# Performance work log

Measured on AMD Instinct MI355X. Metric: run time of the kernel, lower is better.

The kernel has to match this reference:

```python
import jax, jax.numpy as jnp
import numpy as np

B, D, N = 128, 2, 8192
C_CENT, K, R = 32, 32, 0.25
BOTTLE = 8
BN_EPS = 1e-5


def setup_inputs() -> dict:
    key = jax.random.key(0)
    ks = jax.random.split(key, 12)
    w = lambda k, s: jax.random.normal(k, s, dtype=jnp.float32) * 0.05
    z = lambda s: jnp.zeros(s, jnp.float32)
    o = lambda s: jnp.ones(s, jnp.float32)
    return {
        "x": jax.random.normal(ks[0], (B, D, N), dtype=jnp.float32),
        "eps": jax.random.normal(ks[1], (B, BOTTLE), dtype=jnp.float32),
        "sa_c1_w": w(ks[2], (64, D)), "sa_c1_b": z((64,)),
        "sa_bn1_g": o((64,)), "sa_bn1_b": z((64,)),
        "sa_c2_w": w(ks[3], (128, 64)), "sa_c2_b": z((128,)),
        "sa_bn2_g": o((128,)), "sa_bn2_b": z((128,)),
        "sa_c3_w": w(ks[4], (256, 128)), "sa_c3_b": z((256,)),
        "sa_bn3_g": o((256,)), "sa_bn3_b": z((256,)),
        "sa_fc1_w": w(ks[5], (1024, 256 * C_CENT)), "sa_fc1_b": z((1024,)),
        "sa_bn4_g": o((1024,)), "sa_bn4_b": z((1024,)),
        "sa_fc2_w": w(ks[6], (256, 1024)), "sa_fc2_b": z((256,)),
        "sa_bn5_g": o((256,)), "sa_bn5_b": z((256,)),
        "sa_fc3_w": w(ks[7], (BOTTLE, 256)), "sa_fc3_b": z((BOTTLE,)),
        "fce1_w": w(ks[8], (BOTTLE, BOTTLE)), "fce1_b": z((BOTTLE,)),
        "fce2_w": w(ks[9], (BOTTLE, BOTTLE)), "fce2_b": z((BOTTLE,)),
        "dfc1_w": w(ks[10], (32, BOTTLE)), "dfc1_b": z((32,)),
        "dfc2_w": w(ks[11], (128, 32)), "dfc2_b": z((128,)),
        "dfc3_w": w(jax.random.fold_in(key, 99), (512, 128)), "dfc3_b": z((512,)),
    }


def _bn2d(x, g, b):
    m = jnp.mean(x, axis=(0, 2, 3), keepdims=True)
    v = jnp.var(x, axis=(0, 2, 3), keepdims=True)
    return (x - m) * jax.lax.rsqrt(v + BN_EPS) * g[None, :, None, None] + b[None, :, None, None]


def _bn1d(x, g, b):
    m = jnp.mean(x, axis=0, keepdims=True)
    v = jnp.var(x, axis=0, keepdims=True)
    return (x - m) * jax.lax.rsqrt(v + BN_EPS) * g[None, :] + b[None, :]


def _fps(points, n_centroids):
    # points: [B, D, N]; deterministic start at index 0 (torch uses randint)
    c0 = points[:, :, 0]                                   # [B, D]
    dist0 = jnp.sum((c0[:, :, None] - points) ** 2, axis=1)  # [B, N]

    def step(dist, _):
        ind = jnp.argmax(dist, axis=1)                      # [B]
        c = jnp.take_along_axis(points, ind[:, None, None], axis=2)[:, :, 0]  # [B, D]
        dist = jnp.minimum(dist, jnp.sum((c[:, :, None] - points) ** 2, axis=1))
        return dist, c

    _, cs = jax.lax.scan(step, dist0, None, length=n_centroids - 1)  # [C-1, B, D]
    cents = jnp.concatenate([c0[None], cs], axis=0)          # [C, B, D]
    return jnp.transpose(cents, (1, 2, 0))                   # [B, D, C]


def _group_points(points):
    b, _, n = points.shape
    cents = _fps(points, C_CENT)                             # [B, D, C]
    # squared pairwise distances centroid->point: [B, C, N]
    sq = (-2.0 * jnp.einsum('bdc,bdn->bcn', cents, points)
          + jnp.sum(cents ** 2, axis=1)[:, :, None]
          + jnp.sum(points ** 2, axis=1)[:, None, :])
    idx = jnp.broadcast_to(jnp.arange(n, dtype=jnp.int32), (b, C_CENT, n))
    idx = jnp.where(sq > R * R, jnp.int32(n), idx)
    idx = jnp.sort(idx, axis=-1)[:, :, :K]                   # [B, C, K]
    first = idx[:, :, :1]
    idx = jnp.where(idx == n, first, idx)
    bidx = jnp.arange(b)[:, None, None]
    grouped = points[bidx, :, idx]                            # [B, C, K, D]
    return jnp.transpose(grouped, (0, 3, 1, 2))               # [B, D, C, K]


def reference(x, eps, sa_c1_w, sa_c1_b, sa_bn1_g, sa_bn1_b, sa_c2_w, sa_c2_b,
              sa_bn2_g, sa_bn2_b, sa_c3_w, sa_c3_b, sa_bn3_g, sa_bn3_b,
              sa_fc1_w, sa_fc1_b, sa_bn4_g, sa_bn4_b, sa_fc2_w, sa_fc2_b,
              sa_bn5_g, sa_bn5_b, sa_fc3_w, sa_fc3_b, fce1_w, fce1_b,
              fce2_w, fce2_b, dfc1_w, dfc1_b, dfc2_w, dfc2_b, dfc3_w, dfc3_b):
    b = x.shape[0]
    g = _group_points(x)                                     # [B, D, C, K]
    h = jax.nn.relu(_bn2d(jnp.einsum('bdck,od->bock', g, sa_c1_w) + sa_c1_b[None, :, None, None], sa_bn1_g, sa_bn1_b))
    h = jax.nn.relu(_bn2d(jnp.einsum('bdck,od->bock', h, sa_c2_w) + sa_c2_b[None, :, None, None], sa_bn2_g, sa_bn2_b))
    h = jax.nn.relu(_bn2d(jnp.einsum('bdck,od->bock', h, sa_c3_w) + sa_c3_b[None, :, None, None], sa_bn3_g, sa_bn3_b))
    h = jnp.max(h, axis=3)                                   # [B, 256, C]
    h = h.reshape(b, 256 * C_CENT)
    h = jax.nn.relu(_bn1d(h @ sa_fc1_w.T + sa_fc1_b, sa_bn4_g, sa_bn4_b))
    h = jax.nn.relu(_bn1d(h @ sa_fc2_w.T + sa_fc2_b, sa_bn5_g, sa_bn5_b))
    feat = jax.nn.relu(h @ sa_fc3_w.T + sa_fc3_b)            # [B, 8]
    mu = feat @ fce1_w.T + fce1_b
    logvar = feat @ fce2_w.T + fce2_b
    zlat = eps * jnp.exp(0.5 * logvar) + mu                  # reparametrize
    d = jax.nn.relu(zlat @ dfc1_w.T + dfc1_b)
    d = jax.nn.relu(d @ dfc2_w.T + dfc2_b)
    d = d @ dfc3_w.T + dfc3_b
    out = d.reshape(-1, 2, 256)
    return out, mu, logvar
```

## Files before the change

kernel.cpp:

```cpp
#include <hip/hip_runtime.h>
#include <cstdint>
#include <cstddef>

#define NB   128
#define NPT  8192
#define NC   32
#define NK   32
#define MSP  131072
#define R2   0.0625f

typedef unsigned short u16;
typedef unsigned long long u64;
typedef __attribute__((ext_vector_type(8))) short short8v;
typedef __attribute__((ext_vector_type(4))) float f32x4;

static constexpr size_t OFF_CENTS  = 0;
static constexpr size_t OFF_GX     = 8192;
static constexpr size_t OFF_GY     = OFF_GX + 131072;
static constexpr size_t OFF_H1Q    = OFF_GY + 131072;
static constexpr size_t OFF_H2Q    = OFF_H1Q + 4194304;
static constexpr size_t OFF_MAXPRE = OFF_H1Q;
static constexpr size_t OFF_P3S    = OFF_H1Q + 1048576;
static constexpr size_t OFF_P3Q    = OFF_H1Q + 2097152;
static constexpr size_t OFF_PART1  = OFF_H2Q;
static constexpr size_t OFF_PART2  = OFF_H2Q + 4194304;
static constexpr size_t OFF_FC1    = OFF_H2Q + 8388608;
static constexpr size_t OFF_FC2    = OFF_FC1 + 131072;
static constexpr size_t OFF_W2Q    = OFF_FC2 + 32768;
static constexpr size_t OFF_W3Q    = OFF_W2Q + 4096;
static constexpr size_t OFF_PMOM   = OFF_W3Q + 16384;
static constexpr size_t OFF_P2S    = OFF_PMOM + 20480;
static constexpr size_t OFF_P2Q    = OFF_P2S + 131072;
static constexpr size_t OFF_SC1    = OFF_P2Q + 131072;
static constexpr size_t OFF_SH1    = OFF_SC1 + 64;
static constexpr size_t OFF_SC2    = OFF_SH1 + 64;
static constexpr size_t OFF_SH2    = OFF_SC2 + 128;
static constexpr size_t OFF_SC3    = OFF_SH2 + 128;
static constexpr size_t OFF_SH3    = OFF_SC3 + 256;
static constexpr size_t OFF_SC4    = OFF_SH3 + 256;
static constexpr size_t OFF_SH4    = OFF_SC4 + 1024;
static constexpr size_t OFF_SC5    = OFF_SH4 + 1024;
static constexpr size_t OFF_SH5    = OFF_SC5 + 256;
static constexpr size_t OFF_SC3E   = OFF_SH5 + 256;
static constexpr size_t OFF_SH3E   = OFF_SC3E + 8192;

__device__ __forceinline__ u16 f2bf(float f) {
  uint32_t u = __float_as_uint(f);
  u += 0x7FFFu + ((u >> 16) & 1u);
  return (u16)(u >> 16);
}
__device__ __forceinline__ float bf2f(u16 h) {
  return __uint_as_float(((uint32_t)h) << 16);
}
__device__ __forceinline__ void gload16(const void* g, void* l) {
  __builtin_amdgcn_global_load_lds(
      (const __attribute__((address_space(1))) void*)g,
      (__attribute__((address_space(3))) void*)l, 16, 0, 0);
}

__global__ __launch_bounds__(512) void fps_kernel(const float* __restrict__ x,
                                                  float* __restrict__ cents) {
  const int b = blockIdx.x, t = threadIdx.x;
  const int lane = t & 63, wid = t >> 6;
  const float* xb = x + (size_t)b * 2 * NPT;
  float px[16], py[16], dst[16];
  __shared__ float lpx[NPT], lpy[NPT];
  __shared__ u64 slot[2][8];
  __shared__ float cxs[NC], cys[NC];
#pragma unroll
  for (int k = 0; k < 16; k++) {
    const int id = t + k * 512;
    px[k] = xb[id];
    py[k] = xb[NPT + id];
    lpx[id] = px[k];
    lpy[id] = py[k];
  }
  const float c0x = xb[0], c0y = xb[NPT];
  if (t == 0) { cxs[0] = c0x; cys[0] = c0y; }
#pragma unroll
  for (int k = 0; k < 16; k++) {
    const float dx = __fsub_rn(c0x, px[k]);
    const float dy = __fsub_rn(c0y, py[k]);
    dst[k] = __fadd_rn(__fmul_rn(dx, dx), __fmul_rn(dy, dy));
  }
  __syncthreads();
  for (int j = 1; j < NC; j++) {
    u64 v[16];
#pragma unroll
    for (int k = 0; k < 16; k++)
      v[k] = ((u64)__float_as_uint(dst[k]) << 32) | (uint32_t)~(uint32_t)(t + k * 512);
#pragma unroll
    for (int s = 8; s > 0; s >>= 1)
#pragma unroll
      for (int k = 0; k < s; k++)
        if (v[k + s] > v[k]) v[k] = v[k + s];
    u64 best = v[0];
#pragma unroll
    for (int off = 1; off < 64; off <<= 1) {
      const u64 o = __shfl_xor(best, off);
      if (o > best) best = o;
    }
    const int pb = j & 1;
    if (lane == 0) slot[pb][wid] = best;
    __syncthreads();
    u64 w = slot[pb][0];
#pragma unroll
    for (int s = 1; s < 8; s++) {
      const u64 o = slot[pb][s];
      if (o > w) w = o;
    }
    const int wi = (int)~(uint32_t)w;
    const float wx = lpx[wi], wy = lpy[wi];
    if (t == 0) { cxs[j] = wx; cys[j] = wy; }
#pragma unroll
    for (int k = 0; k < 16; k++) {
      const float dx = __fsub_rn(wx, px[k]);
      const float dy = __fsub_rn(wy, py[k]);
      const float nd = __fadd_rn(__fmul_rn(dx, dx), __fmul_rn(dy, dy));
      dst[k] = fminf(dst[k], nd);
    }
  }
  __syncthreads();
  if (t < NC) {
    cents[(size_t)b * 64 + t]      = cxs[t];
    cents[(size_t)b * 64 + 32 + t] = cys[t];
  }
}

__global__ __launch_bounds__(512) void group_kernel(const float* __restrict__ x,
                                                    const float* __restrict__ cents,
                                                    float* __restrict__ gx,
                                                    float* __restrict__ gy,
                                                    float* __restrict__ pmom) {
  const int b  = blockIdx.x & 127;
  const int cg = blockIdx.x >> 7;
  const int t = threadIdx.x;
  const int lane = t & 63, wid = t >> 6;
  const float* px = x + (size_t)b * 2 * NPT;
  const float* py = px + NPT;
  const int p0 = t * 16;

  float lx[16], ly[16], sp[16];
#pragma unroll
  for (int k = 0; k < 16; k += 4) {
    const float4 vx = *(const float4*)(px + p0 + k);
    const float4 vy = *(const float4*)(py + p0 + k);
    lx[k] = vx.x; lx[k + 1] = vx.y; lx[k + 2] = vx.z; lx[k + 3] = vx.w;
    ly[k] = vy.x; ly[k + 1] = vy.y; ly[k + 2] = vy.z; ly[k + 3] = vy.w;
  }
#pragma unroll
  for (int k = 0; k < 16; k++)
    sp[k] = __fadd_rn(__fmul_rn(lx[k], lx[k]), __fmul_rn(ly[k], ly[k]));

  __shared__ int idxs[4][NK];
  __shared__ int wtot[4][8];
  uint32_t mask[4];
  int ebase[4];

#pragma unroll
  for (int c = 0; c < 4; c++) {
    const int cc = cg * 4 + c;
    const float cx = cents[(size_t)b * 64 + cc];
    const float cy = cents[(size_t)b * 64 + 32 + cc];
    const float sc = __fadd_rn(__fmul_rn(cx, cx), __fmul_rn(cy, cy));
    uint32_t m = 0;
#pragma unroll
    for (int k = 0; k < 16; k++) {
      const float dot = __fadd_rn(__fmul_rn(cx, lx[k]), __fmul_rn(cy, ly[k]));
      const float sq  = __fadd_rn(__fadd_rn(__fmul_rn(-2.0f, dot), sc), sp[k]);
      if (!(sq > R2)) m |= (1u << k);
    }
    mask[c] = m;
    const int cnt = (int)__popc(m);
    int pre = cnt;
#pragma unroll
    for (int off = 1; off < 64; off <<= 1) {
      const int o = __shfl_up(pre, off);
      if (lane >= off) pre += o;
    }
    ebase[c] = pre - cnt;
    if (lane == 63) wtot[c][wid] = pre;
  }
  __syncthreads();
#pragma unroll
  for (int c = 0; c < 4; c++) {
    int off = 0;
#pragma unroll
    for (int w = 0; w < 8; w++) off += (w < wid) ? wtot[c][w] : 0;
    int pos = ebase[c] + off;
    uint32_t m = mask[c];
    while (m && pos < NK) {
      const int k = __ffs(m) - 1;
      idxs[c][pos] = p0 + k;
      m &= m - 1;
      pos++;
    }
  }
  __syncthreads();
  if (wid < 4) {
    int tot = 0;
#pragma unroll
    for (int w = 0; w < 8; w++) tot += wtot[wid][w];
    if (lane >= tot && lane < NK) idxs[wid][lane] = idxs[wid][0];
  }
  __syncthreads();
  if (wid < 4) {
    const int bc = b * 32 + cg * 4 + wid;
    float gxv = 0.f, gyv = 0.f;
    if (lane < NK) {
      const int id = idxs[wid][lane];
      gxv = px[id];
      gyv = py[id];
      const size_t s = (size_t)bc * NK + lane;
      gx[s] = gxv;
      gy[s] = gyv;
    }
    float sx = gxv, sy = gyv;
    float sxx = gxv * gxv, syy = gyv * gyv, sxy = gxv * gyv;
#pragma unroll
    for (int off = 1; off < 64; off <<= 1) {
      sx  += __shfl_xor(sx, off);
      sy  += __shfl_xor(sy, off);
      sxx += __shfl_xor(sxx, off);
      syy += __shfl_xor(syy, off);
      sxy += __shfl_xor(sxy, off);
    }
    if (lane == 0) {
      pmom[0 * 4096 + bc] = sx;
      pmom[1 * 4096 + bc] = sy;
      pmom[2 * 4096 + bc] = sxx;
      pmom[3 * 4096 + bc] = syy;
      pmom[4 * 4096 + bc] = sxy;
    }
  }
}

__global__ __launch_bounds__(256) void bn1fin_kernel(const float* __restrict__ pmom,
                                                     const float* __restrict__ w,
                                                     const float* __restrict__ gamma,
                                                     const float* __restrict__ beta,
                                                     float* __restrict__ sc,
                                                     float* __restrict__ sh) {
  const int t = threadIdx.x, lane = t & 63, wid = t >> 6;
  __shared__ float rr[5][4];
  __shared__ float red[5];
#pragma unroll
  for (int m = 0; m < 5; m++) {
    float a = 0.f;
#pragma unroll
    for (int i = 0; i < 4; i++) {
      const float4 v = *(const float4*)(pmom + m * 4096 + (t + i * 256) * 4);
      a += v.x + v.y + v.z + v.w;
    }
#pragma unroll
    for (int off = 1; off < 64; off <<= 1) a += __shfl_xor(a, off);
    if (lane == 0) rr[m][wid] = a;
  }
  __syncthreads();
  if (t == 0) {
#pragma unroll
    for (int m = 0; m < 5; m++) red[m] = rr[m][0] + rr[m][1] + rr[m][2] + rr[m][3];
  }
  __syncthreads();
  if (t < 64) {
    const double invM = 1.0 / (double)MSP;
    const double mx = red[0] * invM, my = red[1] * invM;
    const double exx = red[2] * invM, eyy = red[3] * invM, exy = red[4] * invM;
    const double w0 = w[2 * t], w1 = w[2 * t + 1];
    const double mean = w0 * mx + w1 * my;
    double var = w0 * w0 * (exx - mx * mx) + 2.0 * w0 * w1 * (exy - mx * my)
               + w1 * w1 * (eyy - my * my);
    if (var < 0.0) var = 0.0;
    const double s = (double)gamma[t] / sqrt(var + 1e-5);
    sc[t] = (float)s;
    sh[t] = (float)((double)beta[t] - mean * s);
  }
}

__global__ __launch_bounds__(256) void wquant_kernel(const float* __restrict__ c2w,
                                                     const float* __restrict__ c3w,
                                                     u16* __restrict__ w2q,
                                                     u16* __restrict__ w3qf) {
  const int id = blockIdx.x * 256 + threadIdx.x;
  if (id < 2048) {
    const int e = id * 4;
    const float4 v = *(const float4*)(c2w + e);
    uint2 q;
    q.x = (uint32_t)f2bf(v.x) | ((uint32_t)f2bf(v.y) << 16);
    q.y = (uint32_t)f2bf(v.z) | ((uint32_t)f2bf(v.w) << 16);
    *(uint2*)(w2q + e) = q;
  } else if (id < 2048 + 4096) {
    const int id2 = id - 2048;
    const int oc = id2 >> 4, k8 = (id2 & 15) * 8;
    const float4 v0 = *(const float4*)(c3w + oc * 128 + k8);
    const float4 v1 = *(const float4*)(c3w + oc * 128 + k8 + 4);
    uint4 q;
    q.x = (uint32_t)f2bf(v0.x) | ((uint32_t)f2bf(v0.y) << 16);
    q.y = (uint32_t)f2bf(v0.z) | ((uint32_t)f2bf(v0.w) << 16);
    q.z = (uint32_t)f2bf(v1.x) | ((uint32_t)f2bf(v1.y) << 16);
    q.w = (uint32_t)f2bf(v1.z) | ((uint32_t)f2bf(v1.w) << 16);
    const int off = ((((oc >> 4) * 4 + (k8 >> 5)) * 4 + ((k8 & 31) >> 3)) * 16 + (oc & 15)) * 8;
    *(uint4*)(w3qf + off) = q;
  }
}

__global__ __launch_bounds__(256) void conv1_kernel(const float* __restrict__ gx,
                                                    const float* __restrict__ gy,
                                                    const float* __restrict__ w,
                                                    const float* __restrict__ sc1,
                                                    const float* __restrict__ sh1,
                                                    u16* __restrict__ h1q) {
  const int t = threadIdx.x, blk = blockIdx.x;
  const int base = blk * 256;
  const int sg = t & 31, cg = t >> 5;
  __shared__ float lx[256], ly[256];
  lx[t] = gx[base + t];
  ly[t] = gy[base + t];
  __syncthreads();
  float w0[8], w1[8], scr[8], shr[8];
#pragma unroll
  for (int j = 0; j < 8; j++) {
    w0[j] = w[(cg * 8 + j) * 2];
    w1[j] = w[(cg * 8 + j) * 2 + 1];
    scr[j] = sc1[cg * 8 + j];
    shr[j] = sh1[cg * 8 + j];
  }
#pragma unroll
  for (int i = 0; i < 8; i++) {
    const int pl = sg + i * 32;
    const float xx = lx[pl], yy = ly[pl];
    uint32_t pk[4];
#pragma unroll
    for (int h = 0; h < 4; h++) {
      float v0 = fmaf(w0[2 * h], xx, w1[2 * h] * yy);
      float v1 = fmaf(w0[2 * h + 1], xx, w1[2 * h + 1] * yy);
      v0 = fmaxf(fmaf(v0, scr[2 * h], shr[2 * h]), 0.f);
      v1 = fmaxf(fmaf(v1, scr[2 * h + 1], shr[2 * h + 1]), 0.f);
      pk[h] = (uint32_t)f2bf(v0) | ((uint32_t)f2bf(v1) << 16);
    }
    *(uint4*)(h1q + (size_t)(base + pl) * 64 + cg * 8) = *(uint4*)pk;
  }
}

__global__ __launch_bounds__(256) void finalize_kernel(
    const float* __restrict__ psum, const float* __restrict__ psq,
    int P, float invM,
    const float* __restrict__ gamma, const float* __restrict__ beta,
    float* __restrict__ scale, float* __restrict__ shift,
    float* __restrict__ scexp, float* __restrict__ shexp, int expand) {
  const int c = blockIdx.x, t = threadIdx.x;
  float s = 0.f, q = 0.f;
  for (int p = t; p < P; p += 256) {
    s += psum[(size_t)c * P + p];
    q += psq[(size_t)c * P + p];
  }
#pragma unroll
  for (int off = 1; off < 64; off <<= 1) {
    s += __shfl_xor(s, off);
    q += __shfl_xor(q, off);
  }
  __shared__ float r1[4], r2[4], bc2[2];
  if ((t & 63) == 0) { r1[t >> 6] = s; r2[t >> 6] = q; }
  __syncthreads();
  if (t == 0) {
    s = r1[0] + r1[1] + r1[2] + r1[3];
    q = r2[0] + r2[1] + r2[2] + r2[3];
    const float m = s * invM;
    float v = fmaf(-m, m, q * invM);
    v = fmaxf(v, 0.f);
    const float sc = gamma[c] * (float)(1.0 / sqrt((double)v + 1e-5));
    const float sh = fmaf(-m, sc, beta[c]);
    scale[c] = sc;
    shift[c] = sh;
    bc2[0] = sc;
    bc2[1] = sh;
  }
  __syncthreads();
  if (t < expand) {
    scexp[c * expand + t] = bc2[0];
    shexp[c * expand + t] = bc2[1];
  }
}

__global__ __launch_bounds__(256) void bncol_kernel(
    const float* __restrict__ in, int rows, int cols,
    const float* __restrict__ gamma, const float* __restrict__ beta,
    float* __restrict__ scale, float* __restrict__ shift) {
  const int jl = threadIdx.x & 63;
  const int rg = threadIdx.x >> 6;
  const int j = blockIdx.x * 64 + jl;
  float s = 0.f, q = 0.f;
  for (int r = rg; r < rows; r += 4) {
    const float v = in[(size_t)r * cols + j];
    s += v;
    q = fmaf(v, v, q);
  }
  __shared__ float rs[4][64], rq[4][64];
  rs[rg][jl] = s;
  rq[rg][jl] = q;
  __syncthreads();
  if (rg == 0) {
    s = rs[0][jl] + rs[1][jl] + rs[2][jl] + rs[3][jl];
    q = rq[0][jl] + rq[1][jl] + rq[2][jl] + rq[3][jl];
    const float m = s / (float)rows;
    float var = q / (float)rows - m * m;
    var = fmaxf(var, 0.f);
    const float sc = gamma[j] * (float)(1.0 / sqrt((double)var + 1e-5));
    scale[j] = sc;
    shift[j] = fmaf(-m, sc, beta[j]);
  }
}

template <int K, bool STOREOUT, bool DOMAX, bool TRANS>
__global__ __launch_bounds__(512) void convmfma_kernel(
    const u16* __restrict__ act,
    const u16* __restrict__ wq,
    const float* __restrict__ ascale, const float* __restrict__ ashift,
    u16* __restrict__ outq,
    float* __restrict__ psum, float* __restrict__ psq,
    float* __restrict__ maxpre,
    int OCT) {
  constexpr int OCB = 128, BS = 128;
  constexpr int RB = K * 2;
  constexpr int STAGE = (OCB + BS) * RB;
  constexpr int EPI = (STOREOUT ? BS * OCB * 2 : 0) + 4 * OCB * 2 * 4;
  constexpr int SMEM = STAGE > EPI ? STAGE : EPI;
  __shared__ __align__(16) char smem[SMEM];
  char* Wl = smem;
  char* Bl = smem + OCB * RB;
  const int t = threadIdx.x;
  const int lane = t & 63, wid = t >> 6;
  const int sblk = blockIdx.x;
  const int ocb = blockIdx.y * OCB;
  const int s_base = sblk * BS;

  {
    constexpr int CH = OCB * RB / 16, PW = CH / 8, NI = PW / 64;
#pragma unroll
    for (int j = 0; j < NI; j++) {
      const int c = wid * PW + j * 64 + lane;
      const int b = c * 16;
      const int oc = b / RB;
      const int off = b & (RB - 1);
      gload16((const char*)wq + (size_t)(ocb + oc) * RB + (off ^ ((oc & 7) << 4)),
              Wl + (wid * PW + j * 64) * 16);
    }
  }
  if constexpr (!TRANS) {
    constexpr int CH = BS * RB / 16, PW = CH / 8, NI = PW / 64;
#pragma unroll
    for (int j = 0; j < NI; j++) {
      const int c = wid * PW + j * 64 + lane;
      const int b = c * 16;
      const int sl = b / RB;
      const int off = b & (RB - 1);
      gload16((const char*)act + (size_t)(s_base + sl) * RB + (off ^ ((sl & 7) << 4)),
              Bl + (wid * PW + j * 64) * 16);
    }
  } else {
    const int kk0 = (t & 15) * 8;
    const float4 scA = *(const float4*)(ascale + kk0);
    const float4 scB = *(const float4*)(ascale + kk0 + 4);
    const float4 shA = *(const float4*)(ashift + kk0);
    const float4 shB = *(const float4*)(ashift + kk0 + 4);
    const float scr[8] = {scA.x, scA.y, scA.z, scA.w, scB.x, scB.y, scB.z, scB.w};
    const float shr[8] = {shA.x, shA.y, shA.z, shA.w, shB.x, shB.y, shB.z, shB.w};
    constexpr int NI = BS * K / (512 * 8);
#pragma unroll
    for (int i = 0; i < NI; i++) {
      const int sl = (t >> 4) + i * 32;
      const uint4 raw = *(const uint4*)(act + (size_t)(s_base + sl) * K + kk0);
      const u16* rp = (const u16*)&raw;
      uint32_t pk[4];
#pragma unroll
      for (int h = 0; h < 4; h++) {
        const float f0 = fmaxf(fmaf(bf2f(rp[2 * h]),     scr[2 * h],     shr[2 * h]),     0.f);
        const float f1 = fmaxf(fmaf(bf2f(rp[2 * h + 1]), scr[2 * h + 1], shr[2 * h + 1]), 0.f);
        pk[h] = (uint32_t)f2bf(f0) | ((uint32_t)f2bf(f1) << 16);
      }
      *(uint4*)(Bl + sl * RB + ((kk0 * 2) ^ ((sl & 7) << 4))) = *(uint4*)pk;
    }
  }
  __syncthreads();

  const int wr = wid >> 2, wc = wid & 3;
  const int l15 = lane & 15, l4 = lane >> 4;
  f32x4 acc[4][2];
#pragma unroll
  for (int fo = 0; fo < 4; fo++)
#pragma unroll
    for (int fs = 0; fs < 2; fs++)
#pragma unroll
      for (int q = 0; q < 4; q++) acc[fo][fs][q] = 0.f;

#pragma unroll
  for (int ks = 0; ks < K / 32; ks++) {
    short8v a[4], bv[2];
#pragma unroll
    for (int f = 0; f < 4; f++) {
      const int oc = wr * 64 + f * 16 + l15;
      a[f] = *(const short8v*)(Wl + oc * RB + ((ks * 64 + l4 * 16) ^ ((oc & 7) << 4)));
    }
#pragma unroll
    for (int f = 0; f < 2; f++) {
      const int sl = wc * 32 + f * 16 + l15;
      bv[f] = *(const short8v*)(Bl + sl * RB + ((ks * 64 + l4 * 16) ^ ((sl & 7) << 4)));
    }
#pragma unroll
    for (int fo = 0; fo < 4; fo++)
#pragma unroll
      for (int fs = 0; fs < 2; fs++)
        acc[fo][fs] = __builtin_amdgcn_mfma_f32_16x16x32_bf16(a[fo], bv[fs], acc[fo][fs], 0, 0, 0);
  }
  __syncthreads();

  char* Dl = smem;
  float* sred1 = (float*)(smem + (STOREOUT ? BS * OCB * 2 : 0));
  float* sred2 = sred1 + 4 * OCB;

#pragma unroll
  for (int fo = 0; fo < 4; fo++)
#pragma unroll
    for (int r = 0; r < 4; r++) {
      float s1 = acc[fo][0][r] + acc[fo][1][r];
      float s2 = fmaf(acc[fo][0][r], acc[fo][0][r], acc[fo][1][r] * acc[fo][1][r]);
#pragma unroll
      for (int off = 1; off < 16; off <<= 1) {
        s1 += __shfl_xor(s1, off);
        s2 += __shfl_xor(s2, off);
      }
      if (l15 == 0) {
        const int ocl = wr * 64 + fo * 16 + l4 * 4 + r;
        sred1[wc * OCB + ocl] = s1;
        sred2[wc * OCB + ocl] = s2;
      }
    }

  if constexpr (DOMAX) {
#pragma unroll
    for (int fo = 0; fo < 4; fo++)
#pragma unroll
      for (int r = 0; r < 4; r++) {
        float g = fmaxf(acc[fo][0][r], acc[fo][1][r]);
#pragma unroll
        for (int off = 1; off < 16; off <<= 1) g = fmaxf(g, __shfl_xor(g, off));
        if (l15 == 0) {
          const int oc = ocb + wr * 64 + fo * 16 + l4 * 4 + r;
          maxpre[(size_t)oc * 4096 + sblk * 4 + wc] = g;
        }
      }
  }

  if constexpr (STOREOUT) {
#pragma unroll
    for (int fo = 0; fo < 4; fo++)
#pragma unroll
      for (int fs = 0; fs < 2; fs++) {
        const int sl = wc * 32 + fs * 16 + l15;
        const int ocl = wr * 64 + fo * 16 + l4 * 4;
        uint2 q;
        q.x = (uint32_t)f2bf(acc[fo][fs][0]) | ((uint32_t)f2bf(acc[fo][fs][1]) << 16);
        q.y = (uint32_t)f2bf(acc[fo][fs][2]) | ((uint32_t)f2bf(acc[fo][fs][3]) << 16);
        *(uint2*)(Dl + sl * 256 + ((ocl * 2) ^ ((sl & 7) << 4))) = q;
      }
  }
  __syncthreads();

  if (t < OCB) {
    psum[(size_t)(ocb + t) * 1024 + sblk] =
        sred1[t] + sred1[OCB + t] + sred1[2 * OCB + t] + sred1[3 * OCB + t];
    psq[(size_t)(ocb + t) * 1024 + sblk] =
        sred2[t] + sred2[OCB + t] + sred2[2 * OCB + t] + sred2[3 * OCB + t];
  }
  if constexpr (STOREOUT) {
#pragma unroll
    for (int i = 0; i < 4; i++) {
      const int c = t + i * 512;
      const int sl = c >> 4, slot = c & 15;
      const uint4 v = *(const uint4*)(Dl + sl * 256 + ((slot * 16) ^ ((sl & 7) << 4)));
      *(uint4*)(outq + (size_t)(s_base + sl) * OCT + slot * 8) = v;
    }
  }
}

__global__ __launch_bounds__(256) void conv3_kernel(
    const u16* __restrict__ act,
    const u16* __restrict__ wqf,
    const float* __restrict__ ascale, const float* __restrict__ ashift,
    float* __restrict__ psum, float* __restrict__ psq,
    float* __restrict__ maxpre) {
  constexpr int K = 128, RB = 256;
  __shared__ __align__(16) char Bl[64 * RB];
  const int t = threadIdx.x;
  const int lane = t & 63, wid = t >> 6;
  const int ws = wid & 1, wo = wid >> 1;
  const int blk = blockIdx.x;
  const int sblk = blk >> 1;
  const int ocp = (blk & 1) * 128;
  const int l15 = lane & 15, l4 = lane >> 4;
  const int s_base = sblk * 64;

  short8v b[4][4];
  {
    const int ocq0 = (ocp >> 4) + wo * 4;
#pragma unroll
    for (int fo = 0; fo < 4; fo++)
#pragma unroll
      for (int ks = 0; ks < 4; ks++)
        b[fo][ks] = *(const short8v*)(wqf + ((((ocq0 + fo) * 4 + ks) * 4 + l4) * 16 + l15) * 8);
  }

  {
    const int kk0 = (t & 15) * 8;
    const float4 scA = *(const float4*)(ascale + kk0);
    const float4 scB = *(const float4*)(ascale + kk0 + 4);
    const float4 shA = *(const float4*)(ashift + kk0);
    const float4 shB = *(const float4*)(ashift + kk0 + 4);
    const float scr[8] = {scA.x, scA.y, scA.z, scA.w, scB.x, scB.y, scB.z, scB.w};
    const float shr[8] = {shA.x, shA.y, shA.z, shA.w, shB.x, shB.y, shB.z, shB.w};
#pragma unroll
    for (int i = 0; i < 4; i++) {
      const int sl = (t >> 4) + i * 16;
      const uint4 raw = *(const uint4*)(act + (size_t)(s_base + sl) * K + kk0);
      const u16* rp = (const u16*)&raw;
      uint32_t pk[4];
#pragma unroll
      for (int h = 0; h < 4; h++) {
        const float f0 = fmaxf(fmaf(bf2f(rp[2 * h]),     scr[2 * h],     shr[2 * h]),     0.f);
        const float f1 = fmaxf(fmaf(bf2f(rp[2 * h + 1]), scr[2 * h + 1], shr[2 * h + 1]), 0.f);
        pk[h] = (uint32_t)f2bf(f0) | ((uint32_t)f2bf(f1) << 16);
      }
      *(uint4*)(Bl + sl * RB + ((kk0 * 2) ^ ((sl & 7) << 4))) = *(uint4*)pk;
    }
  }
  __syncthreads();

  f32x4 acc[2][4];
#pragma unroll
  for (int fs = 0; fs < 2; fs++)
#pragma unroll
    for (int fo = 0; fo < 4; fo++)
#pragma unroll
      for (int q = 0; q < 4; q++) acc[fs][fo][q] = 0.f;

#pragma unroll
  for (int ks = 0; ks < 4; ks++) {
    short8v a[2];
#pragma unroll
    for (int fs = 0; fs < 2; fs++) {
      const int srow = ws * 32 + fs * 16 + l15;
      a[fs] = *(const short8v*)(Bl + srow * RB + ((ks * 64 + l4 * 16) ^ ((srow & 7) << 4)));
    }
#pragma unroll
    for (int fs = 0; fs < 2; fs++)
#pragma unroll
      for (int fo = 0; fo < 4; fo++)
        acc[fs][fo] = __builtin_amdgcn_mfma_f32_16x16x32_bf16(a[fs], b[fo][ks], acc[fs][fo], 0, 0, 0);
  }

  const int gid = sblk * 2 + ws;
#pragma unroll
  for (int fo = 0; fo < 4; fo++) {
    float s1 = acc[0][fo][0], s2 = acc[0][fo][0] * acc[0][fo][0];
    float mx = acc[0][fo][0];
#pragma unroll
    for (int fs = 0; fs < 2; fs++)
#pragma unroll
      for (int r = 0; r < 4; r++) {
        if (fs == 0 && r == 0) continue;
        const float v = acc[fs][fo][r];
        s1 += v;
        s2 = fmaf(v, v, s2);
        mx = fmaxf(mx, v);
      }
    s1 += __shfl_xor(s1, 16); s1 += __shfl_xor(s1, 32);
    s2 += __shfl_xor(s2, 16); s2 += __shfl_xor(s2, 32);
    mx = fmaxf(mx, __shfl_xor(mx, 16));
    mx = fmaxf(mx, __shfl_xor(mx, 32));
    if (l4 == 0) {
      const int oc = ocp + wo * 64 + fo * 16 + l15;
      psum[(size_t)oc * 4096 + gid] = s1;
      psq [(size_t)oc * 4096 + gid] = s2;
      maxpre[(size_t)oc * 4096 + gid] = mx;
    }
  }
}

template <int KL, bool TRANS, bool GATHER>
__global__ __launch_bounds__(512) void fcmfma_kernel(
    const float* __restrict__ A,
    const float* __restrict__ W,
    const float* __restrict__ ascale, const float* __restrict__ ashift,
    float* __restrict__ part,
    int Ntot, int Ktot) {
  __shared__ __align__(16) char smem[65536];
  char* Wh = smem;
  char* Wl = smem + 16384;
  char* Ah = smem + 32768;
  char* Al = smem + 49152;
  const int t = threadIdx.x;
  const int lane = t & 63, wid = t >> 6;
  const int sblk = blockIdx.x;
  const int n_base = blockIdx.y * 128;
  const int k_begin = sblk * KL;
  const int kq = t & 15;
  const int r0 = t >> 4;
  const int kk = kq * 4;
  const int wn = wid & 1, wm = wid >> 1;
  const int l15 = lane & 15, l4 = lane >> 4;

  f32x4 acc[4][2];
#pragma unroll
  for (int fo = 0; fo < 4; fo++)
#pragma unroll
    for (int fs = 0; fs < 2; fs++)
#pragma unroll
      for (int q = 0; q < 4; q++) acc[fo][fs][q] = 0.f;

  for (int c0 = 0; c0 < KL; c0 += 64) {
    const int kabs = k_begin + c0 + kk;
    float4 tsc, tsh;
    if constexpr (TRANS) {
      tsc = *(const float4*)(ascale + kabs);
      tsh = *(const float4*)(ashift + kabs);
    }
#pragma unroll
    for (int i = 0; i < 4; i++) {
      const int row = r0 + i * 32;
      const int byte = row * 128 + ((kk * 2) ^ ((row & 7) << 4));
      {
        const float4 v = *(const float4*)(W + (size_t)(n_base + row) * Ktot + kabs);
        const u16 h0 = f2bf(v.x), h1 = f2bf(v.y), h2 = f2bf(v.z), h3 = f2bf(v.w);
        uint2 hv, lv;
        hv.x = (uint32_t)h0 | ((uint32_t)h1 << 16);
        hv.y = (uint32_t)h2 | ((uint32_t)h3 << 16);
        lv.x = (uint32_t)f2bf(v.x - bf2f(h0)) | ((uint32_t)f2bf(v.y - bf2f(h1)) << 16);
        lv.y = (uint32_t)f2bf(v.z - bf2f(h2)) | ((uint32_t)f2bf(v.w - bf2f(h3)) << 16);
        *(uint2*)(Wh + byte) = hv;
        *(uint2*)(Wl + byte) = lv;
      }
      {
        float4 v;
        if constexpr (GATHER)
          v = *(const float4*)(A + (size_t)(kabs >> 5) * 4096 + row * 32 + (kabs & 31));
        else
          v = *(const float4*)(A + (size_t)row * Ktot + kabs);
        if constexpr (TRANS) {
          v.x = fmaxf(fmaf(v.x, tsc.x, tsh.x), 0.f);
          v.y = fmaxf(fmaf(v.y, tsc.y, tsh.y), 0.f);
          v.z = fmaxf(fmaf(v.z, tsc.z, tsh.z), 0.f);
          v.w = fmaxf(fmaf(v.w, tsc.w, tsh.w), 0.f);
        }
        const u16 h0 = f2bf(v.x), h1 = f2bf(v.y), h2 = f2bf(v.z), h3 = f2bf(v.w);
        uint2 hv, lv;
        hv.x = (uint32_t)h0 | ((uint32_t)h1 << 16);
        hv.y = (uint32_t)h2 | ((uint32_t)h3 << 16);
        lv.x = (uint32_t)f2bf(v.x - bf2f(h0)) | ((uint32_t)f2bf(v.y - bf2f(h1)) << 16);
        lv.y = (uint32_t)f2bf(v.z - bf2f(h2)) | ((uint32_t)f2bf(v.w - bf2f(h3)) << 16);
        *(uint2*)(Ah + byte) = hv;
        *(uint2*)(Al + byte) = lv;
      }
    }
    __syncthreads();
#pragma unroll
    for (int ks = 0; ks < 2; ks++) {
      short8v ah[4], al_[4], bh[2], bl[2];
#pragma unroll
      for (int f = 0; f < 4; f++) {
        const int r = wn * 64 + f * 16 + l15;
        const int byte = r * 128 + ((ks * 64 + l4 * 16) ^ ((r & 7) << 4));
        ah[f]  = *(const short8v*)(Wh + byte);
        al_[f] = *(const short8v*)(Wl + byte);
      }
#pragma unroll
      for (int f = 0; f < 2; f++) {
        const int r = wm * 32 + f * 16 + l15;
        const int byte = r * 128 + ((ks * 64 + l4 * 16) ^ ((r & 7) << 4));
        bh[f] = *(const short8v*)(Ah + byte);
        bl[f] = *(const short8v*)(Al + byte);
      }
#pragma unroll
      for (int fo = 0; fo < 4; fo++)
#pragma unroll
        for (int fs = 0; fs < 2; fs++) {
          acc[fo][fs] = __builtin_amdgcn_mfma_f32_16x16x32_bf16(ah[fo],  bh[fs], acc[fo][fs], 0, 0, 0);
          acc[fo][fs] = __builtin_amdgcn_mfma_f32_16x16x32_bf16(ah[fo],  bl[fs], acc[fo][fs], 0, 0, 0);
          acc[fo][fs] = __builtin_amdgcn_mfma_f32_16x16x32_bf16(al_[fo], bh[fs], acc[fo][fs], 0, 0, 0);
        }
    }
    __syncthreads();
  }
#pragma unroll
  for (int fo = 0; fo < 4; fo++) {
    const int n0 = n_base + wn * 64 + fo * 16 + l4 * 4;
#pragma unroll
    for (int fs = 0; fs < 2; fs++) {
      const int m = wm * 32 + fs * 16 + l15;
      *(float4*)(part + ((size_t)sblk * 128 + m) * Ntot + n0) =
          make_float4(acc[fo][fs][0], acc[fo][fs][1], acc[fo][fs][2], acc[fo][fs][3]);
    }
  }
}

__global__ __launch_bounds__(256) void fcreduce_kernel(const float* __restrict__ part,
                                                       float* __restrict__ out,
                                                       int total, int S) {
  const int id = blockIdx.x * 256 + threadIdx.x;
  if (id >= total) return;
  float s = 0.f;
  for (int p = 0; p < S; p++) s += part[(size_t)p * total + id];
  out[id] = s;
}

__global__ __launch_bounds__(64) void tail_kernel(
    const float* __restrict__ fc2raw, const float* __restrict__ scale5, const float* __restrict__ shift5,
    const float* __restrict__ w3, const float* __restrict__ b3,
    const float* __restrict__ e1w, const float* __restrict__ e1b,
    const float* __restrict__ e2w, const float* __restrict__ e2b,
    const float* __restrict__ eps,
    const float* __restrict__ d1w, const float* __restrict__ d1b,
    const float* __restrict__ d2w, const float* __restrict__ d2b,
    const float* __restrict__ d3w, const float* __restrict__ d3b,
    float* __restrict__ out) {
  const int b = blockIdx.x, t = threadIdx.x;
  __shared__ float h5[256], feat[8], z[8], d1[32], d2[128];
  for (int i = t; i < 256; i += 64) {
    const float v = fc2raw[(size_t)b * 256 + i];
    h5[i] = fmaxf(fmaf(v, scale5[i], shift5[i]), 0.f);
  }
  __syncthreads();
  if (t < 8) {
    float s = b3[t];
    for (int i = 0; i < 256; i++) s = fmaf(h5[i], w3[t * 256 + i], s);
    feat[t] = fmaxf(s, 0.f);
  }
  __syncthreads();
  if (t < 8) {
    float mu = e1b[t], lv = e2b[t];
    for (int j = 0; j < 8; j++) {
      mu = fmaf(feat[j], e1w[t * 8 + j], mu);
      lv = fmaf(feat[j], e2w[t * 8 + j], lv);
    }
    out[65536 + b * 8 + t] = mu;
    out[66560 + b * 8 + t] = lv;
    z[t] = fmaf(eps[b * 8 + t], expf(0.5f * lv), mu);
  }
  __syncthreads();
  if (t < 32) {
    float s = d1b[t];
    for (int j = 0; j < 8; j++) s = fmaf(z[j], d1w[t * 8 + j], s);
    d1[t] = fmaxf(s, 0.f);
  }
  __syncthreads();
  for (int o = t; o < 128; o += 64) {
    float s = d2b[o];
    for (int j = 0; j < 32; j++) s = fmaf(d1[j], d2w[o * 32 + j], s);
    d2[o] = fmaxf(s, 0.f);
  }
  __syncthreads();
  for (int o = t; o < 512; o += 64) {
    float s = d3b[o];
    for (int j = 0; j < 128; j++) s = fmaf(d2[j], d3w[o * 128 + j], s);
    out[(size_t)b * 512 + o] = s;
  }
}

extern "C" void kernel_launch(void* const* d_in, const int* in_sizes, int n_in,
                              void* d_out, int out_size, void* d_ws, size_t ws_size,
                              hipStream_t stream) {
  const float* x    = (const float*)d_in[0];
  const float* eps  = (const float*)d_in[1];
  const float* c1w  = (const float*)d_in[2];
  const float* bn1g = (const float*)d_in[4];
  const float* bn1b = (const float*)d_in[5];
  const float* c2w  = (const float*)d_in[6];
  const float* bn2g = (const float*)d_in[8];
  const float* bn2b = (const float*)d_in[9];
  const float* c3w  = (const float*)d_in[10];
  const float* bn3g = (const float*)d_in[12];
  const float* bn3b = (const float*)d_in[13];
  const float* f1w  = (const float*)d_in[14];
  const float* bn4g = (const float*)d_in[16];
  const float* bn4b = (const float*)d_in[17];
  const float* f2w  = (const float*)d_in[18];
  const float* bn5g = (const float*)d_in[20];
  const float* bn5b = (const float*)d_in[21];
  const float* f3w  = (const float*)d_in[22];
  const float* f3b  = (const float*)d_in[23];
  const float* e1w  = (const float*)d_in[24];
  const float* e1b  = (const float*)d_in[25];
  const float* e2w  = (const float*)d_in[26];
  const float* e2b  = (const float*)d_in[27];
  const float* d1w  = (const float*)d_in[28];
  const float* d1b  = (const float*)d_in[29];
  const float* d2w  = (const float*)d_in[30];
  const float* d2b  = (const float*)d_in[31];
  const float* d3w  = (const float*)d_in[32];
  const float* d3b  = (const float*)d_in[33];

  float* ws = (float*)d_ws;
  float* cents  = ws + OFF_CENTS;
  float* gx     = ws + OFF_GX;
  float* gy     = ws + OFF_GY;
  u16*   h1q    = (u16*)(ws + OFF_H1Q);
  u16*   h2q    = (u16*)(ws + OFF_H2Q);
  u16*   w2q    = (u16*)(ws + OFF_W2Q);
  u16*   w3qf   = (u16*)(ws + OFF_W3Q);
  float* pmom   = ws + OFF_PMOM;
  float* maxpre = ws + OFF_MAXPRE;
  float* part1  = ws + OFF_PART1;
  float* part2  = ws + OFF_PART2;
  float* fc1o   = ws + OFF_FC1;
  float* fc2o   = ws + OFF_FC2;
  float* p2s = ws + OFF_P2S, *p2q = ws + OFF_P2Q;
  float* p3s = ws + OFF_P3S, *p3q = ws + OFF_P3Q;
  float* sc1 = ws + OFF_SC1, *sh1 = ws + OFF_SH1;
  float* sc2 = ws + OFF_SC2, *sh2 = ws + OFF_SH2;
  float* sc3 = ws + OFF_SC3, *sh3 = ws + OFF_SH3;
  float* sc4 = ws + OFF_SC4, *sh4 = ws + OFF_SH4;
  float* sc5 = ws + OFF_SC5, *sh5 = ws + OFF_SH5;
  float* sc3e = ws + OFF_SC3E, *sh3e = ws + OFF_SH3E;

  wquant_kernel<<<24, 256, 0, stream>>>(c2w, c3w, w2q, w3qf);
  fps_kernel<<<NB, 512, 0, stream>>>(x, cents);
  group_kernel<<<1024, 512, 0, stream>>>(x, cents, gx, gy, pmom);

  bn1fin_kernel<<<1, 256, 0, stream>>>(pmom, c1w, bn1g, bn1b, sc1, sh1);
  conv1_kernel<<<512, 256, 0, stream>>>(gx, gy, c1w, sc1, sh1, h1q);

  convmfma_kernel<64, true, false, false><<<dim3(1024, 1), 512, 0, stream>>>(
      h1q, w2q, nullptr, nullptr, h2q, p2s, p2q, nullptr, 128);
  finalize_kernel<<<128, 256, 0, stream>>>(p2s, p2q, 1024, 1.f / MSP, bn2g, bn2b,
                                           sc2, sh2, nullptr, nullptr, 0);

  conv3_kernel<<<4096, 256, 0, stream>>>(h2q, w3qf, sc2, sh2, p3s, p3q, maxpre);
  finalize_kernel<<<256, 256, 0, stream>>>(p3s, p3q, 4096, 1.f / MSP, bn3g, bn3b,
                                           sc3, sh3, sc3e, sh3e, 32);

  fcmfma_kernel<256, true, true><<<dim3(32, 8), 512, 0, stream>>>(
      maxpre, f1w, sc3e, sh3e, part1, 1024, 8192);
  fcreduce_kernel<<<512, 256, 0, stream>>>(part1, fc1o, 131072, 32);
  bncol_kernel<<<16, 256, 0, stream>>>(fc1o, 128, 1024, bn4g, bn4b, sc4, sh4);

  fcmfma_kernel<128, true, false><<<dim3(8, 2), 512, 0, stream>>>(
      fc1o, f2w, sc4, sh4, part2, 256, 1024);
  fcreduce_kernel<<<128, 256, 0, stream>>>(part2, fc2o, 32768, 8);
  bncol_kernel<<<4, 256, 0, stream>>>(fc2o, 128, 256, bn5g, bn5b, sc5, sh5);

  tail_kernel<<<NB, 64, 0, stream>>>(fc2o, sc5, sh5, f3w, f3b, e1w, e1b, e2w, e2b, eps,
                                     d1w, d1b, d2w, d2b, d3w, d3b, (float*)d_out);
}
```

Baseline: 221.7 us.

## Fuse conv1 into conv2 MFMA kernel and widen conv3 blocks to all channels

```diff
diff --git a/kernel.cpp b/kernel.cpp
--- a/kernel.cpp
+++ b/kernel.cpp
@@ -304,44 +304,6 @@
   }
 }
 
-__global__ __launch_bounds__(256) void conv1_kernel(const float* __restrict__ gx,
-                                                    const float* __restrict__ gy,
-                                                    const float* __restrict__ w,
-                                                    const float* __restrict__ sc1,
-                                                    const float* __restrict__ sh1,
-                                                    u16* __restrict__ h1q) {
-  const int t = threadIdx.x, blk = blockIdx.x;
-  const int base = blk * 256;
-  const int sg = t & 31, cg = t >> 5;
-  __shared__ float lx[256], ly[256];
-  lx[t] = gx[base + t];
-  ly[t] = gy[base + t];
-  __syncthreads();
-  float w0[8], w1[8], scr[8], shr[8];
-#pragma unroll
-  for (int j = 0; j < 8; j++) {
-    w0[j] = w[(cg * 8 + j) * 2];
-    w1[j] = w[(cg * 8 + j) * 2 + 1];
-    scr[j] = sc1[cg * 8 + j];
-    shr[j] = sh1[cg * 8 + j];
-  }
-#pragma unroll
-  for (int i = 0; i < 8; i++) {
-    const int pl = sg + i * 32;
-    const float xx = lx[pl], yy = ly[pl];
-    uint32_t pk[4];
-#pragma unroll
-    for (int h = 0; h < 4; h++) {
-      float v0 = fmaf(w0[2 * h], xx, w1[2 * h] * yy);
-      float v1 = fmaf(w0[2 * h + 1], xx, w1[2 * h + 1] * yy);
-      v0 = fmaxf(fmaf(v0, scr[2 * h], shr[2 * h]), 0.f);
-      v1 = fmaxf(fmaf(v1, scr[2 * h + 1], shr[2 * h + 1]), 0.f);
-      pk[h] = (uint32_t)f2bf(v0) | ((uint32_t)f2bf(v1) << 16);
-    }
-    *(uint4*)(h1q + (size_t)(base + pl) * 64 + cg * 8) = *(uint4*)pk;
-  }
-}
-
 __global__ __launch_bounds__(256) void finalize_kernel(
     const float* __restrict__ psum, const float* __restrict__ psq,
     int P, float invM,
@@ -411,28 +373,34 @@
   }
 }
 
-template <int K, bool STOREOUT, bool DOMAX, bool TRANS>
-__global__ __launch_bounds__(512) void convmfma_kernel(
-    const u16* __restrict__ act,
+__global__ __launch_bounds__(512) void conv2fused_kernel(
+    const float* __restrict__ gx, const float* __restrict__ gy,
+    const float* __restrict__ w1,
+    const float* __restrict__ sc1, const float* __restrict__ sh1,
     const u16* __restrict__ wq,
-    const float* __restrict__ ascale, const float* __restrict__ ashift,
     u16* __restrict__ outq,
-    float* __restrict__ psum, float* __restrict__ psq,
-    float* __restrict__ maxpre,
-    int OCT) {
-  constexpr int OCB = 128, BS = 128;
+    float* __restrict__ psum, float* __restrict__ psq) {
+  constexpr int K = 64, OCB = 128, BS = 128, OCT = 128;
   constexpr int RB = K * 2;
   constexpr int STAGE = (OCB + BS) * RB;
-  constexpr int EPI = (STOREOUT ? BS * OCB * 2 : 0) + 4 * OCB * 2 * 4;
+  constexpr int EPI = BS * OCB * 2 + 4 * OCB * 2 * 4;
   constexpr int SMEM = STAGE > EPI ? STAGE : EPI;
-  __shared__ __align__(16) char smem[SMEM];
+  __shared__ __align__(16) char smem[SMEM + 1024];
   char* Wl = smem;
   char* Bl = smem + OCB * RB;
+  float* par = (float*)(smem + SMEM);
   const int t = threadIdx.x;
   const int lane = t & 63, wid = t >> 6;
   const int sblk = blockIdx.x;
-  const int ocb = blockIdx.y * OCB;
   const int s_base = sblk * BS;
+
+  if (t < 64) {
+    par[t]       = w1[t * 2];
+    par[64 + t]  = w1[t * 2 + 1];
+    par[128 + t] = sc1[t];
+    par[192 + t] = sh1[t];
+  }
+  __syncthreads();
 
   {
     constexpr int CH = OCB * RB / 16, PW = CH / 8, NI = PW / 64;
@@ -442,44 +410,26 @@
       const int b = c * 16;
       const int oc = b / RB;
       const int off = b & (RB - 1);
-      gload16((const char*)wq + (size_t)(ocb + oc) * RB + (off ^ ((oc & 7) << 4)),
+      gload16((const char*)wq + (size_t)oc * RB + (off ^ ((oc & 7) << 4)),
               Wl + (wid * PW + j * 64) * 16);
     }
   }
-  if constexpr (!TRANS) {
-    constexpr int CH = BS * RB / 16, PW = CH / 8, NI = PW / 64;
-#pragma unroll
-    for (int j = 0; j < NI; j++) {
-      const int c = wid * PW + j * 64 + lane;
-      const int b = c * 16;
-      const int sl = b / RB;
-      const int off = b & (RB - 1);
-      gload16((const char*)act + (size_t)(s_base + sl) * RB + (off ^ ((sl & 7) << 4)),
-              Bl + (wid * PW + j * 64) * 16);
-    }
-  } else {
-    const int kk0 = (t & 15) * 8;
-    const float4 scA = *(const float4*)(ascale + kk0);
-    const float4 scB = *(const float4*)(ascale + kk0 + 4);
-    const float4 shA = *(const float4*)(ashift + kk0);
-    const float4 shB = *(const float4*)(ashift + kk0 + 4);
-    const float scr[8] = {scA.x, scA.y, scA.z, scA.w, scB.x, scB.y, scB.z, scB.w};
-    const float shr[8] = {shA.x, shA.y, shA.z, shA.w, shB.x, shB.y, shB.z, shB.w};
-    constexpr int NI = BS * K / (512 * 8);
-#pragma unroll
-    for (int i = 0; i < NI; i++) {
-      const int sl = (t >> 4) + i * 32;
-      const uint4 raw = *(const uint4*)(act + (size_t)(s_base + sl) * K + kk0);
-      const u16* rp = (const u16*)&raw;
-      uint32_t pk[4];
-#pragma unroll
-      for (int h = 0; h < 4; h++) {
-        const float f0 = fmaxf(fmaf(bf2f(rp[2 * h]),     scr[2 * h],     shr[2 * h]),     0.f);
-        const float f1 = fmaxf(fmaf(bf2f(rp[2 * h + 1]), scr[2 * h + 1], shr[2 * h + 1]), 0.f);
-        pk[h] = (uint32_t)f2bf(f0) | ((uint32_t)f2bf(f1) << 16);
-      }
-      *(uint4*)(Bl + sl * RB + ((kk0 * 2) ^ ((sl & 7) << 4))) = *(uint4*)pk;
-    }
+  {
+    const int sl = t >> 2;
+    const int cq = t & 3;
+    const float xx = gx[s_base + sl], yy = gy[s_base + sl];
+    uint32_t pk[8];
+#pragma unroll
+    for (int h = 0; h < 8; h++) {
+      const int c = cq * 16 + 2 * h;
+      float v0 = fmaf(par[c],     xx, par[64 + c]     * yy);
+      float v1 = fmaf(par[c + 1], xx, par[64 + c + 1] * yy);
+      v0 = fmaxf(fmaf(v0, par[128 + c],     par[192 + c]),     0.f);
+      v1 = fmaxf(fmaf(v1, par[128 + c + 1], par[192 + c + 1]), 0.f);
+      pk[h] = (uint32_t)f2bf(v0) | ((uint32_t)f2bf(v1) << 16);
+    }
+    *(uint4*)(Bl + sl * RB + ((cq * 32)      ^ ((sl & 7) << 4))) = *(uint4*)&pk[0];
+    *(uint4*)(Bl + sl * RB + ((cq * 32 + 16) ^ ((sl & 7) << 4))) = *(uint4*)&pk[4];
   }
   __syncthreads();
 
@@ -515,7 +465,7 @@
   __syncthreads();
 
   char* Dl = smem;
-  float* sred1 = (float*)(smem + (STOREOUT ? BS * OCB * 2 : 0));
+  float* sred1 = (float*)(smem + BS * OCB * 2);
   float* sred2 = sred1 + 4 * OCB;
 
 #pragma unroll
@@ -536,54 +486,35 @@
       }
     }
 
-  if constexpr (DOMAX) {
-#pragma unroll
-    for (int fo = 0; fo < 4; fo++)
-#pragma unroll
-      for (int r = 0; r < 4; r++) {
-        float g = fmaxf(acc[fo][0][r], acc[fo][1][r]);
-#pragma unroll
-        for (int off = 1; off < 16; off <<= 1) g = fmaxf(g, __shfl_xor(g, off));
-        if (l15 == 0) {
-          const int oc = ocb + wr * 64 + fo * 16 + l4 * 4 + r;
-          maxpre[(size_t)oc * 4096 + sblk * 4 + wc] = g;
-        }
-      }
-  }
-
-  if constexpr (STOREOUT) {
-#pragma unroll
-    for (int fo = 0; fo < 4; fo++)
-#pragma unroll
-      for (int fs = 0; fs < 2; fs++) {
-        const int sl = wc * 32 + fs * 16 + l15;
-        const int ocl = wr * 64 + fo * 16 + l4 * 4;
-        uint2 q;
-        q.x = (uint32_t)f2bf(acc[fo][fs][0]) | ((uint32_t)f2bf(acc[fo][fs][1]) << 16);
-        q.y = (uint32_t)f2bf(acc[fo][fs][2]) | ((uint32_t)f2bf(acc[fo][fs][3]) << 16);
-        *(uint2*)(Dl + sl * 256 + ((ocl * 2) ^ ((sl & 7) << 4))) = q;
-      }
-  }
+#pragma unroll
+  for (int fo = 0; fo < 4; fo++)
+#pragma unroll
+    for (int fs = 0; fs < 2; fs++) {
+      const int sl = wc * 32 + fs * 16 + l15;
+      const int ocl = wr * 64 + fo * 16 + l4 * 4;
+      uint2 q;
+      q.x = (uint32_t)f2bf(acc[fo][fs][0]) | ((uint32_t)f2bf(acc[fo][fs][1]) << 16);
+      q.y = (uint32_t)f2bf(acc[fo][fs][2]) | ((uint32_t)f2bf(acc[fo][fs][3]) << 16);
+      *(uint2*)(Dl + sl * 256 + ((ocl * 2) ^ ((sl & 7) << 4))) = q;
+    }
   __syncthreads();
 
   if (t < OCB) {
-    psum[(size_t)(ocb + t) * 1024 + sblk] =
+    psum[(size_t)t * 1024 + sblk] =
         sred1[t] + sred1[OCB + t] + sred1[2 * OCB + t] + sred1[3 * OCB + t];
-    psq[(size_t)(ocb + t) * 1024 + sblk] =
+    psq[(size_t)t * 1024 + sblk] =
         sred2[t] + sred2[OCB + t] + sred2[2 * OCB + t] + sred2[3 * OCB + t];
   }
-  if constexpr (STOREOUT) {
-#pragma unroll
-    for (int i = 0; i < 4; i++) {
-      const int c = t + i * 512;
-      const int sl = c >> 4, slot = c & 15;
-      const uint4 v = *(const uint4*)(Dl + sl * 256 + ((slot * 16) ^ ((sl & 7) << 4)));
-      *(uint4*)(outq + (size_t)(s_base + sl) * OCT + slot * 8) = v;
-    }
-  }
-}
-
-__global__ __launch_bounds__(256) void conv3_kernel(
+#pragma unroll
+  for (int i = 0; i < 4; i++) {
+    const int c = t + i * 512;
+    const int sl = c >> 4, slot = c & 15;
+    const uint4 v = *(const uint4*)(Dl + sl * 256 + ((slot * 16) ^ ((sl & 7) << 4)));
+    *(uint4*)(outq + (size_t)(s_base + sl) * OCT + slot * 8) = v;
+  }
+}
+
+__global__ __launch_bounds__(512) void conv3_kernel(
     const u16* __restrict__ act,
     const u16* __restrict__ wqf,
     const float* __restrict__ ascale, const float* __restrict__ ashift,
@@ -594,15 +525,13 @@
   const int t = threadIdx.x;
   const int lane = t & 63, wid = t >> 6;
   const int ws = wid & 1, wo = wid >> 1;
-  const int blk = blockIdx.x;
-  const int sblk = blk >> 1;
-  const int ocp = (blk & 1) * 128;
+  const int sblk = blockIdx.x;
   const int l15 = lane & 15, l4 = lane >> 4;
   const int s_base = sblk * 64;
 
   short8v b[4][4];
   {
-    const int ocq0 = (ocp >> 4) + wo * 4;
+    const int ocq0 = wo * 4;
 #pragma unroll
     for (int fo = 0; fo < 4; fo++)
 #pragma unroll
@@ -619,8 +548,8 @@
     const float scr[8] = {scA.x, scA.y, scA.z, scA.w, scB.x, scB.y, scB.z, scB.w};
     const float shr[8] = {shA.x, shA.y, shA.z, shA.w, shB.x, shB.y, shB.z, shB.w};
 #pragma unroll
-    for (int i = 0; i < 4; i++) {
-      const int sl = (t >> 4) + i * 16;
+    for (int i = 0; i < 2; i++) {
+      const int sl = (t >> 4) + i * 32;
       const uint4 raw = *(const uint4*)(act + (size_t)(s_base + sl) * K + kk0);
       const u16* rp = (const u16*)&raw;
       uint32_t pk[4];
@@ -678,7 +607,7 @@
     mx = fmaxf(mx, __shfl_xor(mx, 16));
     mx = fmaxf(mx, __shfl_xor(mx, 32));
     if (l4 == 0) {
-      const int oc = ocp + wo * 64 + fo * 16 + l15;
+      const int oc = wo * 64 + fo * 16 + l15;
       psum[(size_t)oc * 4096 + gid] = s1;
       psq [(size_t)oc * 4096 + gid] = s2;
       maxpre[(size_t)oc * 4096 + gid] = mx;
@@ -902,7 +831,6 @@
   float* cents  = ws + OFF_CENTS;
   float* gx     = ws + OFF_GX;
   float* gy     = ws + OFF_GY;
-  u16*   h1q    = (u16*)(ws + OFF_H1Q);
   u16*   h2q    = (u16*)(ws + OFF_H2Q);
   u16*   w2q    = (u16*)(ws + OFF_W2Q);
   u16*   w3qf   = (u16*)(ws + OFF_W3Q);
@@ -926,14 +854,13 @@
   group_kernel<<<1024, 512, 0, stream>>>(x, cents, gx, gy, pmom);
 
   bn1fin_kernel<<<1, 256, 0, stream>>>(pmom, c1w, bn1g, bn1b, sc1, sh1);
-  conv1_kernel<<<512, 256, 0, stream>>>(gx, gy, c1w, sc1, sh1, h1q);
-
-  convmfma_kernel<64, true, false, false><<<dim3(1024, 1), 512, 0, stream>>>(
-      h1q, w2q, nullptr, nullptr, h2q, p2s, p2q, nullptr, 128);
+
+  conv2fused_kernel<<<1024, 512, 0, stream>>>(gx, gy, c1w, sc1, sh1, w2q,
+                                              h2q, p2s, p2q);
   finalize_kernel<<<128, 256, 0, stream>>>(p2s, p2q, 1024, 1.f / MSP, bn2g, bn2b,
                                            sc2, sh2, nullptr, nullptr, 0);
 
-  conv3_kernel<<<4096, 256, 0, stream>>>(h2q, w3qf, sc2, sh2, p3s, p3q, maxpre);
+  conv3_kernel<<<2048, 512, 0, stream>>>(h2q, w3qf, sc2, sh2, p3s, p3q, maxpre);
   finalize_kernel<<<256, 256, 0, stream>>>(p3s, p3q, 4096, 1.f / MSP, bn3g, bn3b,
                                            sc3, sh3, sc3e, sh3e, 32);
 
```

New measurement: 214.2 us. -3.4%, faster.
